# Kernel tuning notes

Measured on AMD Instinct MI355X. Metric: run time of the kernel, lower is better.

## Reference

```python
import jax, jax.numpy as jnp
import numpy as np

B, S = 1, 2048
HID, INTER = 4096, 11008
HEADS, HD = 32, 128
GS = 128
EPS = 1e-6
BASE = 10000.0
IMIN, IMAX = -(2**31), 2**31 - 1


def _rope_tables():
    inv_freq = 1.0 / (BASE ** (np.arange(0, HD, 2, dtype=np.float32) / HD))
    t = np.arange(S, dtype=np.float32)
    freqs = np.outer(t, inv_freq)            # [S, HD/2]
    emb = np.concatenate([freqs, freqs], -1)  # [S, HD]
    return jnp.asarray(np.sin(emb), jnp.float32), jnp.asarray(np.cos(emb), jnp.float32)


def setup_inputs() -> dict:
    key = jax.random.key(0)
    ks = iter(jax.random.split(key, 40))
    def qset(in_f, out_f):
        qw = jax.random.randint(next(ks), (in_f // 8, out_f), IMIN, IMAX, dtype=jnp.int32)
        qz = jax.random.randint(next(ks), (in_f // GS, out_f // 8), IMIN, IMAX, dtype=jnp.int32)
        sc = jax.random.uniform(next(ks), (in_f // GS, out_f), dtype=jnp.float32) * 0.01 + 1e-3
        return qw, qz, sc
    dims = {"q": (HID, HID), "k": (HID, HID), "v": (HID, HID), "o": (HID, HID),
            "gate": (HID, INTER), "up": (HID, INTER), "down": (INTER, HID)}
    inp = {}
    for name, (i, o) in dims.items():
        qw, qz, sc = qset(i, o)
        inp["qw_" + name] = qw
        inp["qz_" + name] = qz
        inp["sc_" + name] = sc
    inp["hidden_states"] = jax.random.normal(next(ks), (B, S, HID), dtype=jnp.float32)
    inp["ln1_w"] = jnp.ones((HID,), jnp.float32)
    inp["ln2_w"] = jnp.ones((HID,), jnp.float32)
    sin, cos = _rope_tables()
    inp["sin"] = sin
    inp["cos"] = cos
    # causal additive mask, as stored in ExLlamaBuffer.attn_mask (past_len = 0)
    mask = jnp.where(jnp.tril(jnp.ones((S, S), bool)), 0.0, -1e9).astype(jnp.float32)
    inp["attn_mask"] = mask[None, None]
    return inp


def _dequant(qw, qz, sc):
    # GPTQ int4: qweight [in/8, out] packs 8 rows per int32; qzeros [groups, out/8]
    in_f, out_f = qw.shape[0] * 8, qw.shape[1]
    groups = sc.shape[0]
    sh = jnp.arange(8, dtype=jnp.int32) * 4
    w = ((qw[:, None, :] >> sh[None, :, None]) & 15)
    w = w.reshape(groups, in_f // groups, out_f).astype(jnp.float32)
    z = ((qz[:, :, None] >> sh[None, None, :]) & 15).reshape(groups, out_f).astype(jnp.float32)
    return ((w - (z + 1.0)[:, None, :]) * sc[:, None, :]).reshape(in_f, out_f)


def _rms(x, w):
    v = jnp.mean(x * x, axis=-1, keepdims=True)
    return x * jax.lax.rsqrt(v + EPS) * w


def _rot_half(x):
    x1, x2 = jnp.split(x, 2, axis=-1)
    return jnp.concatenate([-x2, x1], axis=-1)


def reference(qw_q, qz_q, sc_q, qw_k, qz_k, sc_k, qw_v, qz_v, sc_v,
              qw_o, qz_o, sc_o, qw_gate, qz_gate, sc_gate,
              qw_up, qz_up, sc_up, qw_down, qz_down, sc_down,
              hidden_states, ln1_w, ln2_w, sin, cos, attn_mask):
    lin = lambda x, a, b, c: x @ _dequant(a, b, c)
    h = hidden_states
    # attention block
    x = _rms(h, ln1_w)
    q = lin(x, qw_q, qz_q, sc_q).reshape(B, S, HEADS, HD).transpose(0, 2, 1, 3)
    k = lin(x, qw_k, qz_k, sc_k).reshape(B, S, HEADS, HD).transpose(0, 2, 1, 3)
    v = lin(x, qw_v, qz_v, sc_v).reshape(B, S, HEADS, HD).transpose(0, 2, 1, 3)
    c, s = cos[None, None], sin[None, None]  # [1,1,S,HD]
    q = q * c + _rot_half(q) * s
    k = k * c + _rot_half(k) * s
    scores = jnp.einsum('bhqd,bhkd->bhqk', q, k) / np.float32(np.sqrt(HD)) + attn_mask
    p = jax.nn.softmax(scores, axis=-1)
    o = jnp.einsum('bhqk,bhkd->bhqd', p, v).transpose(0, 2, 1, 3).reshape(B, S, HID)
    h = h + lin(o, qw_o, qz_o, sc_o)
    # MLP block
    x = _rms(h, ln2_w)
    y = jax.nn.silu(lin(x, qw_gate, qz_gate, sc_gate)) * lin(x, qw_up, qz_up, sc_up)
    return h + lin(y, qw_down, qz_down, sc_down)
```

## Files before the change

kernel.cpp:

```cpp
#include <hip/hip_runtime.h>
#include <cstdint>
#include <cstddef>

#define S_LEN 2048
#define HID   4096
#define INTER 11008
#define NHEADS 32
#define HD    128

typedef __attribute__((ext_vector_type(4))) float    f32x4;
typedef __attribute__((ext_vector_type(8))) _Float16 f16x8;
typedef __attribute__((ext_vector_type(2))) _Float16 h2;
typedef __attribute__((ext_vector_type(8))) short    s16x8;
typedef __attribute__((ext_vector_type(4))) short    s16x4;
typedef __attribute__((ext_vector_type(4))) unsigned u32x4;

__device__ __forceinline__ float h2f(short s) {
  return (float)__builtin_bit_cast(_Float16, s);
}
__device__ __forceinline__ short f2h(float f) {
  return __builtin_bit_cast(short, (_Float16)f);
}
__device__ __forceinline__ f32x4 mfma16f(s16x8 a, s16x8 b, f32x4 c) {
  return __builtin_amdgcn_mfma_f32_16x16x32_f16(
      __builtin_bit_cast(f16x8, a), __builtin_bit_cast(f16x8, b), c, 0, 0, 0);
}
__device__ __forceinline__ void gload_lds16(const void* g, void* l) {
  __builtin_amdgcn_global_load_lds(
      (const __attribute__((address_space(1))) void*)g,
      (__attribute__((address_space(3))) void*)l, 16, 0, 0);
}

__global__ __launch_bounds__(256) void rmsnorm_kernel(const float* __restrict__ x,
                                                      const float* __restrict__ w,
                                                      short* __restrict__ out) {
  int row = blockIdx.x;
  const float* xr = x + (size_t)row * HID;
  short* orow = out + (size_t)row * HID;
  int tid = threadIdx.x;
  f32x4 v[4];
  float ss = 0.f;
#pragma unroll
  for (int i = 0; i < 4; ++i) {
    v[i] = ((const f32x4*)xr)[i * 256 + tid];
    ss += v[i][0] * v[i][0] + v[i][1] * v[i][1] + v[i][2] * v[i][2] + v[i][3] * v[i][3];
  }
#pragma unroll
  for (int off = 32; off > 0; off >>= 1) ss += __shfl_xor(ss, off);
  __shared__ float psum[4];
  if ((tid & 63) == 0) psum[tid >> 6] = ss;
  __syncthreads();
  float tot = psum[0] + psum[1] + psum[2] + psum[3];
  float r = rsqrtf(tot * (1.0f / (float)HID) + 1e-6f);
#pragma unroll
  for (int i = 0; i < 4; ++i) {
    int base = (i * 256 + tid) * 4;
    s16x4 o;
#pragma unroll
    for (int j = 0; j < 4; ++j) o[j] = f2h(v[i][j] * r * w[base + j]);
    *(s16x4*)&orow[base] = o;
  }
}

template <int OMODE>
__global__ __launch_bounds__(256) void paired_kernel(
    const short* __restrict__ A, int lda,
    const short* __restrict__ BT, int ldb,
    void* __restrict__ Cv, int ldc,
    const float* __restrict__ base, int Kext,
    int gnx, int gny,
    const int* __restrict__ qw, const int* __restrict__ qz,
    const float* __restrict__ sc, short* __restrict__ wt,
    int N, int noff, int dnx, int dqld) {
  __shared__ short sm[4 * 4096];
  int bid = blockIdx.x;
  int gtot = gnx * gny;
  int tid = threadIdx.x;
  if (bid < gtot) {
    int cpx = gtot >> 3;
    int swz = (bid & 7) * cpx + (bid >> 3);
    int bn = swz % gnx, bm = swz / gnx;
    int lane = tid & 63, wv = tid >> 6;
    int wr = wv >> 1, wc = wv & 1;
    f32x4 acc[4][4] = {};
    int nk = Kext >> 5;
    int lr = lane >> 2, lc = lane & 3;
    const short* Abase = A + (size_t)(bm * 128) * lda;
    const short* Bbase = BT + (size_t)(bn * 128) * ldb;
    short* As0 = sm;
    short* Bs0 = sm + 8192;

    auto stage = [&](int buf, int t) {
      int k0 = t << 5;
#pragma unroll
      for (int i = 0; i < 2; ++i) {
        int r = i * 64 + wv * 16 + lr;
        gload_lds16(Abase + (size_t)r * lda + k0 + lc * 8, As0 + buf * 4096 + i * 2048 + wv * 512);
        gload_lds16(Bbase + (size_t)r * ldb + k0 + lc * 8, Bs0 + buf * 4096 + i * 2048 + wv * 512);
      }
    };
    auto compute = [&](int buf) {
      int kc = (lane >> 4) * 8;
      int ra = wr * 64 + (lane & 15);
      int rb = wc * 64 + (lane & 15);
      s16x8 af[4], bfr[4];
#pragma unroll
      for (int m = 0; m < 4; ++m) af[m] = *(const s16x8*)&As0[buf * 4096 + (ra + m * 16) * 32 + kc];
#pragma unroll
      for (int n = 0; n < 4; ++n) bfr[n] = *(const s16x8*)&Bs0[buf * 4096 + (rb + n * 16) * 32 + kc];
#pragma unroll
      for (int m = 0; m < 4; ++m)
#pragma unroll
        for (int n = 0; n < 4; ++n) acc[m][n] = mfma16f(af[m], bfr[n], acc[m][n]);
    };

    stage(0, 0);
    __syncthreads();
    for (int t = 0; t < nk; ++t) {
      if (t + 1 < nk) stage((t + 1) & 1, t + 1);
      compute(t & 1);
      __syncthreads();
    }

    int row0 = bm * 128 + wr * 64 + ((lane >> 4) << 2);
    int col0 = bn * 128 + wc * 64 + (lane & 15);
#pragma unroll
    for (int m = 0; m < 4; ++m)
#pragma unroll
      for (int n = 0; n < 4; ++n)
#pragma unroll
        for (int j = 0; j < 4; ++j) {
          size_t idx = (size_t)(row0 + m * 16 + j) * ldc + col0 + n * 16;
          if (OMODE == 0)      ((short*)Cv)[idx] = f2h(acc[m][n][j]);
          else if (OMODE == 1) ((float*)Cv)[idx] = base[idx] + acc[m][n][j];
          else if (OMODE == 2) ((float*)Cv)[idx] = ((float*)Cv)[idx] + acc[m][n][j];
          else {
            short* C = (short*)Cv;
            float g = h2f(C[idx]);
            float sl = g / (1.f + __expf(-g));
            C[idx] = f2h(sl * acc[m][n][j]);
          }
        }
  } else {
    int id = bid - gtot;
    int n0 = (id % dnx) * 64;
    int k0 = (id / dnx) * 64;
    int g = k0 >> 7;
    int qr0 = k0 >> 3;
#pragma unroll
    for (int i = 0; i < 2; ++i) {
      int idx = tid + i * 256;
      int r = idx >> 6;
      int n = idx & 63;
      int gc = noff + n0 + n;
      unsigned q = (unsigned)qw[(size_t)(qr0 + r) * N + gc];
      float s = sc[(size_t)g * N + gc];
      unsigned zq = (unsigned)qz[(size_t)g * (N >> 3) + (gc >> 3)];
      int z = (int)((zq >> ((gc & 7) * 4)) & 15u);
      _Float16 hz = (_Float16)(float)(1025 + z);
      _Float16 hs = (_Float16)s;
      h2 zc = {hz, hz}, s2 = {hs, hs};
      u32x4 ov;
#pragma unroll
      for (int j = 0; j < 4; ++j) {
        unsigned u = q >> (8 * j);
        unsigned pb = (u & 0xFu) | ((u & 0xF0u) << 12) | 0x64006400u;
        h2 w = __builtin_bit_cast(h2, pb);
        h2 rr = (w - zc) * s2;
        ov[j] = __builtin_bit_cast(unsigned, rr);
      }
      *(u32x4*)&sm[n * 72 + r * 8] = ov;
    }
    __syncthreads();
    int n = tid >> 2;
#pragma unroll
    for (int i = 0; i < 2; ++i) {
      int c = (tid & 3) + i * 4;
      *(s16x8*)&wt[(size_t)(n0 + n) * dqld + k0 + c * 8] = *(const s16x8*)&sm[n * 72 + c * 8];
    }
  }
}

__global__ __launch_bounds__(128) void rope_kernel(short* __restrict__ q, short* __restrict__ k,
                                                   const float* __restrict__ sp,
                                                   const float* __restrict__ cp) {
  int s = blockIdx.x, h = blockIdx.y;
  short* p = (blockIdx.z ? k : q) + (size_t)s * HID + h * HD;
  int d = threadIdx.x;
  float x = h2f(p[d]);
  float xp = h2f(p[d ^ 64]);
  float rot = (d < 64) ? -xp : xp;
  float y = x * cp[s * HD + d] + rot * sp[s * HD + d];
  __syncthreads();
  p[d] = f2h(y);
}

__global__ __launch_bounds__(256, 2) void attn_kernel(const short* __restrict__ qb,
                                                      const short* __restrict__ kb,
                                                      const short* __restrict__ vb,
                                                      short* __restrict__ ob) {
  int qt = (int)(gridDim.x - 1) - blockIdx.x;
  int h = blockIdx.y;
  int tid = threadIdx.x, lane = tid & 63, wv = tid >> 6;
  __shared__ short Kl[64 * 128];
  __shared__ short Vl[128 * 72];
  __shared__ short Pl[4][32 * 72];
  int q0 = qt * 128 + wv * 32;
  s16x8 qf[2][4];
#pragma unroll
  for (int m = 0; m < 2; ++m)
#pragma unroll
    for (int kf = 0; kf < 4; ++kf) {
      int r = q0 + m * 16 + (lane & 15);
      int d = kf * 32 + (lane >> 4) * 8;
      qf[m][kf] = *(const s16x8*)&qb[(size_t)r * HID + h * HD + d];
    }
  f32x4 o[2][8] = {};
  float mrow[2][4], lrow[2][4];
#pragma unroll
  for (int m = 0; m < 2; ++m)
#pragma unroll
    for (int j = 0; j < 4; ++j) { mrow[m][j] = -1e30f; lrow[m][j] = 0.f; }

  auto load_tile = [&](int kv0, s16x8* kr, s16x8* vr) {
#pragma unroll
    for (int i = 0; i < 4; ++i) {
      int cid = tid + i * 256;
      int kv = cid >> 4, c = cid & 15;
      kr[i] = *(const s16x8*)(kb + (size_t)(kv0 + kv) * HID + h * HD + c * 8);
      vr[i] = *(const s16x8*)(vb + (size_t)(kv0 + kv) * HID + h * HD + c * 8);
    }
  };
  auto store_tile = [&](const s16x8* kr, const s16x8* vr) {
#pragma unroll
    for (int i = 0; i < 4; ++i) {
      int cid = tid + i * 256;
      int kv = cid >> 4, c = cid & 15;
      *(s16x8*)((char*)Kl + kv * 256 + ((c ^ (kv & 7)) * 16)) = kr[i];
      int kvs = kv ^ ((c & 7) << 3);
#pragma unroll
      for (int j = 0; j < 8; ++j) Vl[(c * 8 + j) * 72 + kvs] = vr[i][j];
    }
  };

  const float scale = 0.08838834764831845f;
  int kv_end = qt * 128 + 128;
  s16x8 kra[4], vra[4], krb[4], vrb[4];
  load_tile(0, kra, vra);
  store_tile(kra, vra);
  __syncthreads();
  for (int kv0 = 0; kv0 < kv_end; kv0 += 64) {
    bool more = kv0 + 64 < kv_end;
    if (more) load_tile(kv0 + 64, krb, vrb);

    f32x4 sfr[2][4] = {};
    __builtin_amdgcn_s_setprio(1);
#pragma unroll
    for (int nf = 0; nf < 4; ++nf) {
      s16x8 kfr[4];
      int kvr = nf * 16 + (lane & 15);
#pragma unroll
      for (int kf = 0; kf < 4; ++kf) {
        int cc = (kf * 4 + (lane >> 4)) ^ (kvr & 7);
        kfr[kf] = *(const s16x8*)((const char*)Kl + kvr * 256 + cc * 16);
      }
#pragma unroll
      for (int m = 0; m < 2; ++m)
#pragma unroll
        for (int kf = 0; kf < 4; ++kf) sfr[m][nf] = mfma16f(qf[m][kf], kfr[kf], sfr[m][nf]);
    }
    __builtin_amdgcn_s_setprio(0);
#pragma unroll
    for (int m = 0; m < 2; ++m)
#pragma unroll
      for (int j = 0; j < 4; ++j) {
        int qrow = q0 + m * 16 + (lane >> 4) * 4 + j;
        float pm = -1e30f;
#pragma unroll
        for (int nf = 0; nf < 4; ++nf) {
          int kvc = kv0 + nf * 16 + (lane & 15);
          float v = sfr[m][nf][j] * scale;
          v = (kvc <= qrow) ? v : -1e30f;
          sfr[m][nf][j] = v;
          pm = fmaxf(pm, v);
        }
#pragma unroll
        for (int off = 1; off < 16; off <<= 1) pm = fmaxf(pm, __shfl_xor(pm, off));
        float mnew = fmaxf(mrow[m][j], pm);
        float alpha = __expf(mrow[m][j] - mnew);
        mrow[m][j] = mnew;
        float rs = 0.f;
#pragma unroll
        for (int nf = 0; nf < 4; ++nf) {
          float pv = __expf(sfr[m][nf][j] - mnew);
          sfr[m][nf][j] = pv;
          rs += pv;
        }
#pragma unroll
        for (int off = 1; off < 16; off <<= 1) rs += __shfl_xor(rs, off);
        lrow[m][j] = lrow[m][j] * alpha + rs;
#pragma unroll
        for (int nd = 0; nd < 8; ++nd) o[m][nd][j] *= alpha;
      }
#pragma unroll
    for (int m = 0; m < 2; ++m)
#pragma unroll
      for (int nf = 0; nf < 4; ++nf)
#pragma unroll
        for (int j = 0; j < 4; ++j)
          Pl[wv][(m * 16 + (lane >> 4) * 4 + j) * 72 + nf * 16 + (lane & 15)] =
              f2h(sfr[m][nf][j]);
    s16x8 pa[2][2];
#pragma unroll
    for (int m = 0; m < 2; ++m)
#pragma unroll
      for (int kf = 0; kf < 2; ++kf)
        pa[m][kf] = *(const s16x8*)&Pl[wv][(m * 16 + (lane & 15)) * 72 + kf * 32 + (lane >> 4) * 8];
    __builtin_amdgcn_s_setprio(1);
#pragma unroll
    for (int nd = 0; nd < 8; ++nd) {
      s16x8 vf[2];
      int drow = nd * 16 + (lane & 15);
      int key = ((drow >> 3) & 7) << 3;
#pragma unroll
      for (int kf = 0; kf < 2; ++kf)
        vf[kf] = *(const s16x8*)&Vl[drow * 72 + ((kf * 32 + (lane >> 4) * 8) ^ key)];
#pragma unroll
      for (int m = 0; m < 2; ++m)
#pragma unroll
        for (int kf = 0; kf < 2; ++kf) o[m][nd] = mfma16f(pa[m][kf], vf[kf], o[m][nd]);
    }
    __builtin_amdgcn_s_setprio(0);
    __syncthreads();
    if (more) store_tile(krb, vrb);
    __syncthreads();
  }
#pragma unroll
  for (int m = 0; m < 2; ++m)
#pragma unroll
    for (int nd = 0; nd < 8; ++nd)
#pragma unroll
      for (int j = 0; j < 4; ++j) {
        int r = q0 + m * 16 + (lane >> 4) * 4 + j;
        int c = h * HD + nd * 16 + (lane & 15);
        ob[(size_t)r * HID + c] = f2h(o[m][nd][j] / lrow[m][j]);
      }
}

extern "C" void kernel_launch(void* const* d_in, const int* in_sizes, int n_in,
                              void* d_out, int out_size, void* d_ws, size_t ws_size,
                              hipStream_t stream) {
  const int* qw[7]; const int* qz[7]; const float* sc[7];
  for (int i = 0; i < 7; ++i) {
    qw[i] = (const int*)d_in[i * 3 + 0];
    qz[i] = (const int*)d_in[i * 3 + 1];
    sc[i] = (const float*)d_in[i * 3 + 2];
  }
  const float* hin  = (const float*)d_in[21];
  const float* ln1  = (const float*)d_in[22];
  const float* ln2  = (const float*)d_in[23];
  const float* sinp = (const float*)d_in[24];
  const float* cosp = (const float*)d_in[25];
  float* out = (float*)d_out;

  char* ws = (char*)d_ws;
  const size_t MB = 1024 * 1024;
  short* XB    = (short*)(ws);
  short* WA    = (short*)(ws + 16 * MB);
  short* WB    = (short*)(ws + 48 * MB);
  short* KB    = (short*)(ws + 80 * MB);
  short* VB    = (short*)(ws + 96 * MB);
  short* OB    = (short*)(ws + 112 * MB);
  short* GATEB = (short*)(ws + 80 * MB);
  short* QBd   = (short*)d_out;

  dim3 blk(256);

  rmsnorm_kernel<<<S_LEN, blk, 0, stream>>>(hin, ln1, XB);
  paired_kernel<0><<<4096, blk, 0, stream>>>(nullptr, 0, nullptr, 0, nullptr, 0, nullptr, 0,
                                             0, 0, qw[0], qz[0], sc[0], WA, HID, 0, 64, HID);
  paired_kernel<0><<<512 + 4096, blk, 0, stream>>>(XB, HID, WA, HID, QBd, HID, nullptr, HID,
                                                   32, 16, qw[1], qz[1], sc[1], WB, HID, 0, 64, HID);
  paired_kernel<0><<<512 + 4096, blk, 0, stream>>>(XB, HID, WB, HID, KB, HID, nullptr, HID,
                                                   32, 16, qw[2], qz[2], sc[2], WA, HID, 0, 64, HID);
  paired_kernel<0><<<512 + 4096, blk, 0, stream>>>(XB, HID, WA, HID, VB, HID, nullptr, HID,
                                                   32, 16, qw[3], qz[3], sc[3], WB, HID, 0, 64, HID);
  rope_kernel<<<dim3(S_LEN, NHEADS, 2), dim3(128), 0, stream>>>(QBd, KB, sinp, cosp);
  attn_kernel<<<dim3(S_LEN / 128, NHEADS), blk, 0, stream>>>(QBd, KB, VB, OB);
  paired_kernel<1><<<512 + 4096, blk, 0, stream>>>(OB, HID, WB, HID, out, HID, hin, HID,
                                                   32, 16, qw[4], qz[4], sc[4], WA, INTER, 0, 64, HID);
  rmsnorm_kernel<<<S_LEN, blk, 0, stream>>>(out, ln2, XB);

  paired_kernel<0><<<512 + 4096, blk, 0, stream>>>(XB, HID, WA, HID, GATEB + 0, INTER, nullptr, HID,
                                                   32, 16, qw[5], qz[5], sc[5], WB, INTER, 0, 64, HID);
  paired_kernel<3><<<512 + 4096, blk, 0, stream>>>(XB, HID, WB, HID, GATEB + 0, INTER, nullptr, HID,
                                                   32, 16, qw[4], qz[4], sc[4], WA, INTER, 4096, 64, HID);
  paired_kernel<0><<<512 + 4096, blk, 0, stream>>>(XB, HID, WA, HID, GATEB + 4096, INTER, nullptr, HID,
                                                   32, 16, qw[5], qz[5], sc[5], WB, INTER, 4096, 64, HID);
  paired_kernel<3><<<512 + 2816, blk, 0, stream>>>(XB, HID, WB, HID, GATEB + 4096, INTER, nullptr, HID,
                                                   32, 16, qw[4], qz[4], sc[4], WA, INTER, 8192, 44, HID);
  paired_kernel<0><<<352 + 2816, blk, 0, stream>>>(XB, HID, WA, HID, GATEB + 8192, INTER, nullptr, HID,
                                                   22, 16, qw[5], qz[5], sc[5], WB, INTER, 8192, 44, HID);
  paired_kernel<3><<<352 + 4096, blk, 0, stream>>>(XB, HID, WB, HID, GATEB + 8192, INTER, nullptr, HID,
                                                   22, 16, qw[6], qz[6], sc[6], WA, HID, 0, 64, 4096);
  paired_kernel<2><<<512 + 4096, blk, 0, stream>>>(GATEB + 0, INTER, WA, 4096, out, HID, nullptr, 4096,
                                                   32, 16,
                                                   qw[6] + (size_t)(4096 >> 3) * HID,
                                                   qz[6] + (size_t)(4096 >> 7) * (HID / 8),
                                                   sc[6] + (size_t)(4096 >> 7) * HID,
                                                   WB, HID, 0, 64, 4096);
  paired_kernel<2><<<512 + 2816, blk, 0, stream>>>(GATEB + 4096, INTER, WB, 4096, out, HID, nullptr, 4096,
                                                   32, 16,
                                                   qw[6] + (size_t)(8192 >> 3) * HID,
                                                   qz[6] + (size_t)(8192 >> 7) * (HID / 8),
                                                   sc[6] + (size_t)(8192 >> 7) * HID,
                                                   WA, HID, 0, 64, 2816);
  paired_kernel<2><<<512, blk, 0, stream>>>(GATEB + 8192, INTER, WA, 2816, out, HID, nullptr, 2816,
                                            32, 16, nullptr, nullptr, nullptr, nullptr, HID, 0, 1, HID);
}
```

Measured before the change: 1.416 ms.

## Enlarge GEMM tile to 256x128 with 512 threads and simplify dequant path

The fused GEMM/dequant kernel now runs 512 threads (8 waves) per block. Each block computes a 256x128 output tile, so every staged B tile is reused across twice as many A rows and the GEMM grid is halved. The dequant blocks now have each thread unpack one packed int32 word and write 8 halves straight to global memory, which drops the LDS transpose and its barrier. In exchange, the GEMM launches fewer blocks, which can hurt load balance across CUs. Each block also needs more LDS and registers, which may limit how many blocks fit on a CU at once.

```diff
diff --git a/kernel.cpp b/kernel.cpp
--- a/kernel.cpp
+++ b/kernel.cpp
@@ -63,7 +63,7 @@
 }
 
 template <int OMODE>
-__global__ __launch_bounds__(256) void paired_kernel(
+__global__ __launch_bounds__(512) void paired_kernel(
     const short* __restrict__ A, int lda,
     const short* __restrict__ BT, int ldb,
     void* __restrict__ Cv, int ldc,
@@ -72,7 +72,8 @@
     const int* __restrict__ qw, const int* __restrict__ qz,
     const float* __restrict__ sc, short* __restrict__ wt,
     int N, int noff, int dnx, int dqld) {
-  __shared__ short sm[4 * 4096];
+  __shared__ short As[2][256 * 32];
+  __shared__ short Bs[2][128 * 32];
   int bid = blockIdx.x;
   int gtot = gnx * gny;
   int tid = threadIdx.x;
@@ -80,38 +81,38 @@
     int cpx = gtot >> 3;
     int swz = (bid & 7) * cpx + (bid >> 3);
     int bn = swz % gnx, bm = swz / gnx;
-    int lane = tid & 63, wv = tid >> 6;
-    int wr = wv >> 1, wc = wv & 1;
+    int lane = tid & 63, wid = tid >> 6;
+    int wr = wid >> 1, wc = wid & 1;
     f32x4 acc[4][4] = {};
     int nk = Kext >> 5;
-    int lr = lane >> 2, lc = lane & 3;
-    const short* Abase = A + (size_t)(bm * 128) * lda;
+    const short* Abase = A + (size_t)(bm * 256) * lda;
     const short* Bbase = BT + (size_t)(bn * 128) * ldb;
-    short* As0 = sm;
-    short* Bs0 = sm + 8192;
 
     auto stage = [&](int buf, int t) {
       int k0 = t << 5;
 #pragma unroll
       for (int i = 0; i < 2; ++i) {
-        int r = i * 64 + wv * 16 + lr;
-        gload_lds16(Abase + (size_t)r * lda + k0 + lc * 8, As0 + buf * 4096 + i * 2048 + wv * 512);
-        gload_lds16(Bbase + (size_t)r * ldb + k0 + lc * 8, Bs0 + buf * 4096 + i * 2048 + wv * 512);
+        int rbase = i * 128 + wid * 16;
+        int row = rbase + (lane >> 2);
+        gload_lds16(Abase + (size_t)row * lda + k0 + (lane & 3) * 8, &As[buf][rbase * 32]);
       }
+      int rbase = wid * 16;
+      int row = rbase + (lane >> 2);
+      gload_lds16(Bbase + (size_t)row * ldb + k0 + (lane & 3) * 8, &Bs[buf][rbase * 32]);
     };
     auto compute = [&](int buf) {
       int kc = (lane >> 4) * 8;
       int ra = wr * 64 + (lane & 15);
       int rb = wc * 64 + (lane & 15);
-      s16x8 af[4], bfr[4];
-#pragma unroll
-      for (int m = 0; m < 4; ++m) af[m] = *(const s16x8*)&As0[buf * 4096 + (ra + m * 16) * 32 + kc];
-#pragma unroll
-      for (int n = 0; n < 4; ++n) bfr[n] = *(const s16x8*)&Bs0[buf * 4096 + (rb + n * 16) * 32 + kc];
+      s16x8 af[4], bf[4];
+#pragma unroll
+      for (int m = 0; m < 4; ++m) af[m] = *(const s16x8*)&As[buf][(ra + m * 16) * 32 + kc];
+#pragma unroll
+      for (int n = 0; n < 4; ++n) bf[n] = *(const s16x8*)&Bs[buf][(rb + n * 16) * 32 + kc];
 #pragma unroll
       for (int m = 0; m < 4; ++m)
 #pragma unroll
-        for (int n = 0; n < 4; ++n) acc[m][n] = mfma16f(af[m], bfr[n], acc[m][n]);
+        for (int n = 0; n < 4; ++n) acc[m][n] = mfma16f(af[m], bf[n], acc[m][n]);
     };
 
     stage(0, 0);
@@ -122,7 +123,7 @@
       __syncthreads();
     }
 
-    int row0 = bm * 128 + wr * 64 + ((lane >> 4) << 2);
+    int row0 = bm * 256 + wr * 64 + ((lane >> 4) << 2);
     int col0 = bn * 128 + wc * 64 + (lane & 15);
 #pragma unroll
     for (int m = 0; m < 4; ++m)
@@ -145,39 +146,27 @@
     int id = bid - gtot;
     int n0 = (id % dnx) * 64;
     int k0 = (id / dnx) * 64;
+    int n = tid >> 3;
+    int cc = tid & 7;
+    int gc = noff + n0 + n;
     int g = k0 >> 7;
-    int qr0 = k0 >> 3;
-#pragma unroll
-    for (int i = 0; i < 2; ++i) {
-      int idx = tid + i * 256;
-      int r = idx >> 6;
-      int n = idx & 63;
-      int gc = noff + n0 + n;
-      unsigned q = (unsigned)qw[(size_t)(qr0 + r) * N + gc];
-      float s = sc[(size_t)g * N + gc];
-      unsigned zq = (unsigned)qz[(size_t)g * (N >> 3) + (gc >> 3)];
-      int z = (int)((zq >> ((gc & 7) * 4)) & 15u);
-      _Float16 hz = (_Float16)(float)(1025 + z);
-      _Float16 hs = (_Float16)s;
-      h2 zc = {hz, hz}, s2 = {hs, hs};
-      u32x4 ov;
-#pragma unroll
-      for (int j = 0; j < 4; ++j) {
-        unsigned u = q >> (8 * j);
-        unsigned pb = (u & 0xFu) | ((u & 0xF0u) << 12) | 0x64006400u;
-        h2 w = __builtin_bit_cast(h2, pb);
-        h2 rr = (w - zc) * s2;
-        ov[j] = __builtin_bit_cast(unsigned, rr);
-      }
-      *(u32x4*)&sm[n * 72 + r * 8] = ov;
-    }
-    __syncthreads();
-    int n = tid >> 2;
-#pragma unroll
-    for (int i = 0; i < 2; ++i) {
-      int c = (tid & 3) + i * 4;
-      *(s16x8*)&wt[(size_t)(n0 + n) * dqld + k0 + c * 8] = *(const s16x8*)&sm[n * 72 + c * 8];
-    }
+    unsigned q = (unsigned)qw[(size_t)((k0 >> 3) + cc) * N + gc];
+    float s = sc[(size_t)g * N + gc];
+    unsigned zq = (unsigned)qz[(size_t)g * (N >> 3) + (gc >> 3)];
+    int z = (int)((zq >> ((gc & 7) * 4)) & 15u);
+    _Float16 hz = (_Float16)(float)(1025 + z);
+    _Float16 hs = (_Float16)s;
+    h2 zc = {hz, hz}, s2 = {hs, hs};
+    u32x4 ov;
+#pragma unroll
+    for (int j = 0; j < 4; ++j) {
+      unsigned u = q >> (8 * j);
+      unsigned pb = (u & 0xFu) | ((u & 0xF0u) << 12) | 0x64006400u;
+      h2 w = __builtin_bit_cast(h2, pb);
+      h2 rr = (w - zc) * s2;
+      ov[j] = __builtin_bit_cast(unsigned, rr);
+    }
+    *(u32x4*)&wt[(size_t)(n0 + n) * dqld + k0 + cc * 8] = ov;
   }
 }
 
@@ -374,47 +363,47 @@
   short* GATEB = (short*)(ws + 80 * MB);
   short* QBd   = (short*)d_out;
 
-  dim3 blk(256);
-
-  rmsnorm_kernel<<<S_LEN, blk, 0, stream>>>(hin, ln1, XB);
-  paired_kernel<0><<<4096, blk, 0, stream>>>(nullptr, 0, nullptr, 0, nullptr, 0, nullptr, 0,
-                                             0, 0, qw[0], qz[0], sc[0], WA, HID, 0, 64, HID);
-  paired_kernel<0><<<512 + 4096, blk, 0, stream>>>(XB, HID, WA, HID, QBd, HID, nullptr, HID,
-                                                   32, 16, qw[1], qz[1], sc[1], WB, HID, 0, 64, HID);
-  paired_kernel<0><<<512 + 4096, blk, 0, stream>>>(XB, HID, WB, HID, KB, HID, nullptr, HID,
-                                                   32, 16, qw[2], qz[2], sc[2], WA, HID, 0, 64, HID);
-  paired_kernel<0><<<512 + 4096, blk, 0, stream>>>(XB, HID, WA, HID, VB, HID, nullptr, HID,
-                                                   32, 16, qw[3], qz[3], sc[3], WB, HID, 0, 64, HID);
+  dim3 b256(256), b512(512);
+
+  rmsnorm_kernel<<<S_LEN, b256, 0, stream>>>(hin, ln1, XB);
+  paired_kernel<0><<<4096, b512, 0, stream>>>(nullptr, 0, nullptr, 0, nullptr, 0, nullptr, 0,
+                                              0, 0, qw[0], qz[0], sc[0], WA, HID, 0, 64, HID);
+  paired_kernel<0><<<256 + 4096, b512, 0, stream>>>(XB, HID, WA, HID, QBd, HID, nullptr, HID,
+                                                    32, 8, qw[1], qz[1], sc[1], WB, HID, 0, 64, HID);
+  paired_kernel<0><<<256 + 4096, b512, 0, stream>>>(XB, HID, WB, HID, KB, HID, nullptr, HID,
+                                                    32, 8, qw[2], qz[2], sc[2], WA, HID, 0, 64, HID);
+  paired_kernel<0><<<256 + 4096, b512, 0, stream>>>(XB, HID, WA, HID, VB, HID, nullptr, HID,
+                                                    32, 8, qw[3], qz[3], sc[3], WB, HID, 0, 64, HID);
   rope_kernel<<<dim3(S_LEN, NHEADS, 2), dim3(128), 0, stream>>>(QBd, KB, sinp, cosp);
-  attn_kernel<<<dim3(S_LEN / 128, NHEADS), blk, 0, stream>>>(QBd, KB, VB, OB);
-  paired_kernel<1><<<512 + 4096, blk, 0, stream>>>(OB, HID, WB, HID, out, HID, hin, HID,
-                                                   32, 16, qw[4], qz[4], sc[4], WA, INTER, 0, 64, HID);
-  rmsnorm_kernel<<<S_LEN, blk, 0, stream>>>(out, ln2, XB);
-
-  paired_kernel<0><<<512 + 4096, blk, 0, stream>>>(XB, HID, WA, HID, GATEB + 0, INTER, nullptr, HID,
-                                                   32, 16, qw[5], qz[5], sc[5], WB, INTER, 0, 64, HID);
-  paired_kernel<3><<<512 + 4096, blk, 0, stream>>>(XB, HID, WB, HID, GATEB + 0, INTER, nullptr, HID,
-                                                   32, 16, qw[4], qz[4], sc[4], WA, INTER, 4096, 64, HID);
-  paired_kernel<0><<<512 + 4096, blk, 0, stream>>>(XB, HID, WA, HID, GATEB + 4096, INTER, nullptr, HID,
-                                                   32, 16, qw[5], qz[5], sc[5], WB, INTER, 4096, 64, HID);
-  paired_kernel<3><<<512 + 2816, blk, 0, stream>>>(XB, HID, WB, HID, GATEB + 4096, INTER, nullptr, HID,
-                                                   32, 16, qw[4], qz[4], sc[4], WA, INTER, 8192, 44, HID);
-  paired_kernel<0><<<352 + 2816, blk, 0, stream>>>(XB, HID, WA, HID, GATEB + 8192, INTER, nullptr, HID,
-                                                   22, 16, qw[5], qz[5], sc[5], WB, INTER, 8192, 44, HID);
-  paired_kernel<3><<<352 + 4096, blk, 0, stream>>>(XB, HID, WB, HID, GATEB + 8192, INTER, nullptr, HID,
-                                                   22, 16, qw[6], qz[6], sc[6], WA, HID, 0, 64, 4096);
-  paired_kernel<2><<<512 + 4096, blk, 0, stream>>>(GATEB + 0, INTER, WA, 4096, out, HID, nullptr, 4096,
-                                                   32, 16,
-                                                   qw[6] + (size_t)(4096 >> 3) * HID,
-                                                   qz[6] + (size_t)(4096 >> 7) * (HID / 8),
-                                                   sc[6] + (size_t)(4096 >> 7) * HID,
-                                                   WB, HID, 0, 64, 4096);
-  paired_kernel<2><<<512 + 2816, blk, 0, stream>>>(GATEB + 4096, INTER, WB, 4096, out, HID, nullptr, 4096,
-                                                   32, 16,
-                                                   qw[6] + (size_t)(8192 >> 3) * HID,
-                                                   qz[6] + (size_t)(8192 >> 7) * (HID / 8),
-                                                   sc[6] + (size_t)(8192 >> 7) * HID,
-                                                   WA, HID, 0, 64, 2816);
-  paired_kernel<2><<<512, blk, 0, stream>>>(GATEB + 8192, INTER, WA, 2816, out, HID, nullptr, 2816,
-                                            32, 16, nullptr, nullptr, nullptr, nullptr, HID, 0, 1, HID);
-}
+  attn_kernel<<<dim3(S_LEN / 128, NHEADS), b256, 0, stream>>>(QBd, KB, VB, OB);
+  paired_kernel<1><<<256 + 4096, b512, 0, stream>>>(OB, HID, WB, HID, out, HID, hin, HID,
+                                                    32, 8, qw[4], qz[4], sc[4], WA, INTER, 0, 64, HID);
+  rmsnorm_kernel<<<S_LEN, b256, 0, stream>>>(out, ln2, XB);
+
+  paired_kernel<0><<<256 + 4096, b512, 0, stream>>>(XB, HID, WA, HID, GATEB + 0, INTER, nullptr, HID,
+                                                    32, 8, qw[5], qz[5], sc[5], WB, INTER, 0, 64, HID);
+  paired_kernel<3><<<256 + 4096, b512, 0, stream>>>(XB, HID, WB, HID, GATEB + 0, INTER, nullptr, HID,
+                                                    32, 8, qw[4], qz[4], sc[4], WA, INTER, 4096, 64, HID);
+  paired_kernel<0><<<256 + 4096, b512, 0, stream>>>(XB, HID, WA, HID, GATEB + 4096, INTER, nullptr, HID,
+                                                    32, 8, qw[5], qz[5], sc[5], WB, INTER, 4096, 64, HID);
+  paired_kernel<3><<<256 + 2816, b512, 0, stream>>>(XB, HID, WB, HID, GATEB + 4096, INTER, nullptr, HID,
+                                                    32, 8, qw[4], qz[4], sc[4], WA, INTER, 8192, 44, HID);
+  paired_kernel<0><<<176 + 2816, b512, 0, stream>>>(XB, HID, WA, HID, GATEB + 8192, INTER, nullptr, HID,
+                                                    22, 8, qw[5], qz[5], sc[5], WB, INTER, 8192, 44, HID);
+  paired_kernel<3><<<176 + 4096, b512, 0, stream>>>(XB, HID, WB, HID, GATEB + 8192, INTER, nullptr, HID,
+                                                    22, 8, qw[6], qz[6], sc[6], WA, HID, 0, 64, 4096);
+  paired_kernel<2><<<256 + 4096, b512, 0, stream>>>(GATEB + 0, INTER, WA, 4096, out, HID, nullptr, 4096,
+                                                    32, 8,
+                                                    qw[6] + (size_t)(4096 >> 3) * HID,
+                                                    qz[6] + (size_t)(4096 >> 7) * (HID / 8),
+                                                    sc[6] + (size_t)(4096 >> 7) * HID,
+                                                    WB, HID, 0, 64, 4096);
+  paired_kernel<2><<<256 + 2816, b512, 0, stream>>>(GATEB + 4096, INTER, WB, 4096, out, HID, nullptr, 4096,
+                                                    32, 8,
+                                                    qw[6] + (size_t)(8192 >> 3) * HID,
+                                                    qz[6] + (size_t)(8192 >> 7) * (HID / 8),
+                                                    sc[6] + (size_t)(8192 >> 7) * HID,
+                                                    WA, HID, 0, 64, 2816);
+  paired_kernel<2><<<256, b512, 0, stream>>>(GATEB + 8192, INTER, WA, 2816, out, HID, nullptr, 2816,
+                                             32, 8, nullptr, nullptr, nullptr, nullptr, HID, 0, 1, HID);
+}
```

New measurement: 1.719 ms. 21.4% more time.
